# Kernel tuning notes

Hardware: AMD Instinct MI355X
Metric: run time of the kernel (lower is better)

The kernel has to match this reference:

```python
import jax, jax.numpy as jnp
import numpy as np

B, N, D, H, DK, DI = 64, 256, 1024, 8, 64, 2048
NEG = -1e9
SCALE = 1.0 / np.sqrt(DK).astype(np.float32)


def _ln(x, s, b, eps=1e-5):
    m = jnp.mean(x, axis=-1, keepdims=True)
    v = jnp.var(x, axis=-1, keepdims=True)
    return (x - m) * jax.lax.rsqrt(v + eps) * s + b


def _glat_basic(x, mask, npm, wq, wk, wv, wo, bo, ls1, lb1, w1, b1, w2, b2, ls2, lb2):
    # mask: [B,1,N,N] bool, True = blocked
    b, n, d = x.shape
    q = (x @ wq).reshape(b, n, H, DK).transpose(0, 2, 1, 3)  # [B,H,N,DK]
    k = (x @ wk).reshape(b, n, H, DK).transpose(0, 2, 1, 3)
    v = (x @ wv).reshape(b, n, H, DK).transpose(0, 2, 1, 3)
    scores = jnp.einsum('bhqd,bhkd->bhqk', q, k) * SCALE
    scores = jnp.where(mask, NEG, scores)
    attn = jax.nn.softmax(scores, axis=-1)
    out = jnp.einsum('bhqk,bhkd->bhqd', attn, v)
    out = out.transpose(0, 2, 1, 3).reshape(b, n, H * DK)
    out = out @ wo + bo
    out = _ln(out + x, ls1, lb1)           # attn residual + layernorm
    out = out * npm                         # non_pad_mask
    h = jax.nn.relu(out @ w1 + b1) @ w2 + b2
    out2 = _ln(h + out, ls2, lb2) * npm     # FFN residual + layernorm + mask
    return out2


def setup_inputs():
    key = jax.random.key(0)
    ks = jax.random.split(key, 40)
    p = lambda i, shape: jax.random.normal(ks[i], shape, jnp.float32) * 0.02
    inp = {
        'x': jax.random.normal(ks[0], (B, N, D), jnp.float32),
        'adj': jax.random.randint(ks[1], (B, N, N), 0, 2).astype(jnp.int32),
        'non_pad_mask': jnp.ones((B, N, 1), jnp.float32),
        'slf_attn_mask': jnp.zeros((B, N, N), jnp.int32),
    }
    i = 2
    for t in ('g', 'l'):
        inp[f'wq_{t}'] = p(i, (D, H * DK)); i += 1
        inp[f'wk_{t}'] = p(i, (D, H * DK)); i += 1
        inp[f'wv_{t}'] = p(i, (D, H * DK)); i += 1
        inp[f'wo_{t}'] = p(i, (H * DK, D)); i += 1
        inp[f'bo_{t}'] = jnp.zeros((D,), jnp.float32)
        inp[f'ln1s_{t}'] = jnp.ones((D,), jnp.float32)
        inp[f'ln1b_{t}'] = jnp.zeros((D,), jnp.float32)
        inp[f'w1_{t}'] = p(i, (D, DI)); i += 1
        inp[f'b1_{t}'] = jnp.zeros((DI,), jnp.float32)
        inp[f'w2_{t}'] = p(i, (DI, D)); i += 1
        inp[f'b2_{t}'] = jnp.zeros((D,), jnp.float32)
        inp[f'ln2s_{t}'] = jnp.ones((D,), jnp.float32)
        inp[f'ln2b_{t}'] = jnp.zeros((D,), jnp.float32)
    inp['fc_w'] = p(i, (2 * D, D)); i += 1
    inp['fc_b'] = jnp.zeros((D,), jnp.float32)
    return inp


def reference(x, adj, non_pad_mask, slf_attn_mask,
              wq_g, wk_g, wv_g, wo_g, bo_g, ln1s_g, ln1b_g, w1_g, b1_g, w2_g, b2_g, ln2s_g, ln2b_g,
              wq_l, wk_l, wv_l, wo_l, bo_l, ln1s_l, ln1b_l, w1_l, b1_l, w2_l, b2_l, ln2s_l, ln2b_l,
              fc_w, fc_b):
    pad_mask = (slf_attn_mask[:, None, :, :] != 0)            # [B,1,N,N]
    local_mask = pad_mask | (adj[:, None, :, :] == 0)         # local: only attend along edges
    x_g = _glat_basic(x, pad_mask, non_pad_mask,
                      wq_g, wk_g, wv_g, wo_g, bo_g, ln1s_g, ln1b_g,
                      w1_g, b1_g, w2_g, b2_g, ln2s_g, ln2b_g)
    x_l = _glat_basic(x, local_mask, non_pad_mask,
                      wq_l, wk_l, wv_l, wo_l, bo_l, ln1s_l, ln1b_l,
                      w1_l, b1_l, w2_l, b2_l, ln2s_l, ln2b_l)
    out = jnp.concatenate([x_g, x_l], axis=-1) @ fc_w + fc_b
    return out
```

## Files before the change

kernel.cpp:

```cpp
#include <hip/hip_runtime.h>


typedef unsigned short u16;
typedef unsigned long long u64;
typedef __bf16 bf16_t;
typedef bf16_t bf16x8 __attribute__((ext_vector_type(8)));
typedef float  f32x4  __attribute__((ext_vector_type(4)));
typedef u16    u16x8  __attribute__((ext_vector_type(8)));
typedef u16    u16x4  __attribute__((ext_vector_type(4)));

__device__ __forceinline__ float bf2f(u16 u){
  union { unsigned int i; float f; } c; c.i = ((unsigned int)u) << 16; return c.f;
}
__device__ __forceinline__ u16 f2bf(float f){
  union { float f; unsigned int u; } c; c.f = f;
  unsigned int u = c.u;
  unsigned int r = (u + 0x7fffu + ((u >> 16) & 1u)) >> 16;
  return (u16)r;
}

__device__ __forceinline__ void gl16(const u16* g, u16* l){
  __builtin_amdgcn_global_load_lds(
      (const __attribute__((address_space(1))) void*)g,
      (__attribute__((address_space(3))) void*)l, 16, 0, 0);
}

__global__ __launch_bounds__(256) void zero_out(float* out, int n){
  for (int i = blockIdx.x * 256 + threadIdx.x; i < n; i += 256 * 4096) out[i] = 0.f;
}

__global__ __launch_bounds__(256) void cvt_bf16(
    const float* __restrict__ in, u16* __restrict__ out)
{
  const size_t i = ((size_t)blockIdx.x * 256 + threadIdx.x) * 8;
  f32x4 a = *(const f32x4*)&in[i];
  f32x4 b = *(const f32x4*)&in[i + 4];
  u16x8 o;
  #pragma unroll
  for (int j = 0; j < 4; ++j){ o[j] = f2bf(a[j]); o[4+j] = f2bf(b[j]); }
  *(u16x8*)&out[i] = o;
}

__global__ __launch_bounds__(256) void transpose_w(
    const float* __restrict__ src, u16* __restrict__ dst, int K, int N, int dstOff)
{
  __shared__ u16 tile[32][33];
  const int bk = blockIdx.x * 32, bn = blockIdx.y * 32;
  const int t = threadIdx.x;
  const int r = t >> 5, c = t & 31;
  #pragma unroll
  for (int p = 0; p < 4; ++p)
    tile[r + p*8][c] = f2bf(src[(size_t)(bk + r + p*8) * N + bn + c]);
  __syncthreads();
  #pragma unroll
  for (int p = 0; p < 4; ++p)
    dst[(size_t)(dstOff + bn + r + p*8) * K + bk + c] = tile[c][r + p*8];
}

__global__ __launch_bounds__(256) void transpose_w3(
    const float* __restrict__ sA, const float* __restrict__ sB,
    const float* __restrict__ sC, u16* __restrict__ dst, int K, int N)
{
  __shared__ u16 tile[32][33];
  const float* src = blockIdx.z == 0 ? sA : (blockIdx.z == 1 ? sB : sC);
  const int dstOff = blockIdx.z * N;
  const int bk = blockIdx.x * 32, bn = blockIdx.y * 32;
  const int t = threadIdx.x;
  const int r = t >> 5, c = t & 31;
  #pragma unroll
  for (int p = 0; p < 4; ++p)
    tile[r + p*8][c] = f2bf(src[(size_t)(bk + r + p*8) * N + bn + c]);
  __syncthreads();
  #pragma unroll
  for (int p = 0; p < 4; ++p)
    dst[(size_t)(dstOff + bn + r + p*8) * K + bk + c] = tile[c][r + p*8];
}

template<int RELU, int OF32, int ACC>
__global__ __launch_bounds__(512, 2) void gemm256(
    const u16* __restrict__ A0, const u16* __restrict__ A1,
    int Astride, int ksplit,
    const u16* __restrict__ BT, int Bld, int M, int N, int K,
    const float* __restrict__ bias, void* __restrict__ outv, int out_ld)
{
  __shared__ u16 lds[2*32768];
  const int tid  = threadIdx.x;
  const int lane = tid & 63;
  const int wid  = tid >> 6;
  const int wm = wid >> 2, wn = wid & 3;
  const int l15 = lane & 15, l4 = lane >> 4;
  const int m0 = blockIdx.x * 256, n0 = blockIdx.y * 256;

  f32x4 acc[8][4];
  #pragma unroll
  for (int i = 0; i < 8; ++i)
    #pragma unroll
    for (int j = 0; j < 4; ++j)
      acc[i][j] = (f32x4){0.f, 0.f, 0.f, 0.f};

  const int s0 = tid, s1 = tid + 512;
  const int r0 = s0 >> 3, g0 = (s0 & 7) ^ (r0 & 7);
  const int r1 = s1 >> 3, g1 = (s1 & 7) ^ (r1 & 7);

  const int nt = K >> 6;

  auto stageA = [&](int kt, int h, int buf){
    const int kb = kt * 64;
    const u16* Ab = A0; int kl = kb;
    if (kb >= ksplit){ Ab = A1; kl = kb - ksplit; }
    u16* dst = &lds[buf*32768 + h*8192];
    gl16(&Ab[(size_t)(m0 + h*128 + r0) * Astride + kl + g0*8], &dst[s0*8]);
    gl16(&Ab[(size_t)(m0 + h*128 + r1) * Astride + kl + g1*8], &dst[s1*8]);
  };
  auto stageB = [&](int kt, int h, int buf){
    const int kb = kt * 64;
    u16* dst = &lds[buf*32768 + 16384 + h*8192];
    gl16(&BT[(size_t)(n0 + h*128 + r0) * Bld + kb + g0*8], &dst[s0*8]);
    gl16(&BT[(size_t)(n0 + h*128 + r1) * Bld + kb + g1*8], &dst[s1*8]);
  };
  auto lda = [&](int i, int kc, int buf) -> bf16x8 {
    const int r = wm*128 + i*16 + l15;
    const int c = (kc*4 + l4) ^ (r & 7);
    return *(const bf16x8*)&lds[buf*32768 + r*64 + c*8];
  };
  auto ldb = [&](int j, int kc, int buf) -> bf16x8 {
    const int r = wn*64 + j*16 + l15;
    const int c = (kc*4 + l4) ^ (r & 7);
    return *(const bf16x8*)&lds[buf*32768 + 16384 + r*64 + c*8];
  };

  stageA(0, 0, 0); stageA(0, 1, 0); stageB(0, 0, 0); stageB(0, 1, 0);

  for (int t = 0; t < nt; ++t){
    const int buf = t & 1, nbuf = buf ^ 1;
    const bool pf = (t + 1 < nt);
    if (pf){
      stageA(t+1, 0, nbuf);
      asm volatile("s_waitcnt vmcnt(2)" ::: "memory");
    } else {
      asm volatile("s_waitcnt vmcnt(0)" ::: "memory");
    }
    __builtin_amdgcn_sched_barrier(0);
    __builtin_amdgcn_s_barrier();
    __builtin_amdgcn_sched_barrier(0);

    bf16x8 a_[4][2], b_[2][2];
    #pragma unroll
    for (int i = 0; i < 4; ++i){ a_[i][0] = lda(i, 0, buf); a_[i][1] = lda(i, 1, buf); }
    #pragma unroll
    for (int j = 0; j < 2; ++j){ b_[j][0] = ldb(j, 0, buf); b_[j][1] = ldb(j, 1, buf); }
    if (pf) stageA(t+1, 1, nbuf);
    __builtin_amdgcn_s_setprio(1);
    #pragma unroll
    for (int i = 0; i < 4; ++i)
      #pragma unroll
      for (int j = 0; j < 2; ++j){
        acc[i][j] = __builtin_amdgcn_mfma_f32_16x16x32_bf16(a_[i][0], b_[j][0], acc[i][j], 0,0,0);
        acc[i][j] = __builtin_amdgcn_mfma_f32_16x16x32_bf16(a_[i][1], b_[j][1], acc[i][j], 0,0,0);
      }
    __builtin_amdgcn_s_setprio(0);
    #pragma unroll
    for (int j = 0; j < 2; ++j){ b_[j][0] = ldb(2+j, 0, buf); b_[j][1] = ldb(2+j, 1, buf); }
    if (pf) stageB(t+1, 0, nbuf);
    __builtin_amdgcn_s_setprio(1);
    #pragma unroll
    for (int i = 0; i < 4; ++i)
      #pragma unroll
      for (int j = 0; j < 2; ++j){
        acc[i][2+j] = __builtin_amdgcn_mfma_f32_16x16x32_bf16(a_[i][0], b_[j][0], acc[i][2+j], 0,0,0);
        acc[i][2+j] = __builtin_amdgcn_mfma_f32_16x16x32_bf16(a_[i][1], b_[j][1], acc[i][2+j], 0,0,0);
      }
    __builtin_amdgcn_s_setprio(0);
    #pragma unroll
    for (int i = 0; i < 4; ++i){ a_[i][0] = lda(4+i, 0, buf); a_[i][1] = lda(4+i, 1, buf); }
    if (pf) stageB(t+1, 1, nbuf);
    __builtin_amdgcn_s_setprio(1);
    #pragma unroll
    for (int i = 0; i < 4; ++i)
      #pragma unroll
      for (int j = 0; j < 2; ++j){
        acc[4+i][2+j] = __builtin_amdgcn_mfma_f32_16x16x32_bf16(a_[i][0], b_[j][0], acc[4+i][2+j], 0,0,0);
        acc[4+i][2+j] = __builtin_amdgcn_mfma_f32_16x16x32_bf16(a_[i][1], b_[j][1], acc[4+i][2+j], 0,0,0);
      }
    __builtin_amdgcn_s_setprio(0);
    #pragma unroll
    for (int j = 0; j < 2; ++j){ b_[j][0] = ldb(j, 0, buf); b_[j][1] = ldb(j, 1, buf); }
    __builtin_amdgcn_s_setprio(1);
    #pragma unroll
    for (int i = 0; i < 4; ++i)
      #pragma unroll
      for (int j = 0; j < 2; ++j){
        acc[4+i][j] = __builtin_amdgcn_mfma_f32_16x16x32_bf16(a_[i][0], b_[j][0], acc[4+i][j], 0,0,0);
        acc[4+i][j] = __builtin_amdgcn_mfma_f32_16x16x32_bf16(a_[i][1], b_[j][1], acc[4+i][j], 0,0,0);
      }
    __builtin_amdgcn_s_setprio(0);

    __builtin_amdgcn_sched_barrier(0);
    __builtin_amdgcn_s_barrier();
    __builtin_amdgcn_sched_barrier(0);
  }

  const int rb = m0 + wm*128 + l4*4;
  const int cb = n0 + wn*64 + l15;
  #pragma unroll
  for (int i = 0; i < 8; ++i){
    #pragma unroll
    for (int j = 0; j < 4; ++j){
      const int col = cb + j*16;
      const float badd = bias ? bias[col] : 0.f;
      #pragma unroll
      for (int r = 0; r < 4; ++r){
        const int row = rb + i*16 + r;
        float y = acc[i][j][r] + badd;
        if (RELU) y = y > 0.f ? y : 0.f;
        if (OF32){
          float* po = &((float*)outv)[(size_t)row * out_ld + col];
          if (ACC) y += *po;
          *po = y;
        } else {
          u16* po = &((u16*)outv)[(size_t)row * out_ld + col];
          if (ACC) y += bf2f(*po);
          *po = f2bf(y);
        }
      }
    }
  }
}

__global__ __launch_bounds__(256) void mask_pack(
    const int* __restrict__ slf, const int* __restrict__ adj,
    u64* __restrict__ mb_g, u64* __restrict__ mb_l)
{
  const int idx  = blockIdx.x * 4 + (threadIdx.x >> 6);
  const int lane = threadIdx.x & 63;
  const size_t mi = (size_t)(idx >> 2) * 256 + (size_t)(idx & 3) * 64 + lane;
  const bool g = slf[mi] != 0;
  const bool l = g || (adj[mi] == 0);
  const u64 bg = __ballot(g);
  const u64 bl = __ballot(l);
  if (lane == 0){ mb_g[idx] = bg; mb_l[idx] = bl; }
}

__global__ __launch_bounds__(256) void attn_mfma(
    const u16* __restrict__ qkv, const u64* __restrict__ mb,
    int boff, u16* __restrict__ out)
{
  __shared__ u16 kbuf[64*64];
  __shared__ u16 vtbuf[64*64];
  __shared__ u16 pbuf[4][32*64];

  const int b_loc = blockIdx.x >> 4;
  const int h     = (blockIdx.x >> 1) & 7;
  const int qt    = blockIdx.x & 1;
  const int b     = boff + b_loc;
  const int t     = threadIdx.x;
  const int w     = t >> 6, lane = t & 63;
  const int l15   = lane & 15, l4 = lane >> 4;

  bf16x8 qf[2][2];
  {
    const int rbase = b_loc*256 + qt*128 + w*32;
    #pragma unroll
    for (int i = 0; i < 2; ++i)
      #pragma unroll
      for (int kc = 0; kc < 2; ++kc)
        qf[i][kc] = *(const bf16x8*)&qkv[(size_t)(rbase + i*16 + l15)*1536 + h*64 + kc*32 + l4*8];
  }

  f32x4 acc_o[2][4];
  float m_[2][4], l_[2][4];
  #pragma unroll
  for (int i = 0; i < 2; ++i){
    #pragma unroll
    for (int j = 0; j < 4; ++j) acc_o[i][j] = (f32x4){0.f,0.f,0.f,0.f};
    #pragma unroll
    for (int r = 0; r < 4; ++r){ m_[i][r] = -1e30f; l_[i][r] = 0.f; }
  }

  for (int c = 0; c < 4; ++c){
    __syncthreads();
    {
      const int kr = t >> 2, dg = (t & 3) * 16;
      const size_t rbase = (size_t)(b_loc*256 + c*64 + kr)*1536 + h*64 + dg;
      u16x8 k0 = *(const u16x8*)&qkv[rbase + 512];
      u16x8 k1 = *(const u16x8*)&qkv[rbase + 512 + 8];
      u16x8 v0 = *(const u16x8*)&qkv[rbase + 1024];
      u16x8 v1 = *(const u16x8*)&qkv[rbase + 1024 + 8];
      const int sw = (kr & 7) << 3;
      *(u16x8*)&kbuf[kr*64 + (dg ^ sw)]       = k0;
      *(u16x8*)&kbuf[kr*64 + ((dg + 8) ^ sw)] = k1;
      #pragma unroll
      for (int e = 0; e < 8; ++e){
        const int d0 = dg + e, d1 = dg + 8 + e;
        vtbuf[d0*64 + (kr ^ ((d0 & 7) << 3))] = v0[e];
        vtbuf[d1*64 + (kr ^ ((d1 & 7) << 3))] = v1[e];
      }
    }
    __syncthreads();

    bf16x8 kfr[4][2];
    #pragma unroll
    for (int jb = 0; jb < 4; ++jb){
      const int key = jb*16 + l15;
      const int sw = (key & 7) << 3;
      #pragma unroll
      for (int kc = 0; kc < 2; ++kc)
        kfr[jb][kc] = *(const bf16x8*)&kbuf[key*64 + ((kc*32 + l4*8) ^ sw)];
    }
    f32x4 s_[2][4];
    #pragma unroll
    for (int i = 0; i < 2; ++i)
      #pragma unroll
      for (int jb = 0; jb < 4; ++jb){
        f32x4 a = (f32x4){0.f,0.f,0.f,0.f};
        a = __builtin_amdgcn_mfma_f32_16x16x32_bf16(qf[i][0], kfr[jb][0], a, 0,0,0);
        a = __builtin_amdgcn_mfma_f32_16x16x32_bf16(qf[i][1], kfr[jb][1], a, 0,0,0);
        s_[i][jb] = a;
      }

    #pragma unroll
    for (int i = 0; i < 2; ++i){
      #pragma unroll
      for (int r = 0; r < 4; ++r){
        const int prow = i*16 + l4*4 + r;
        const int qrow = qt*128 + w*32 + prow;
        const u64 bits = mb[((size_t)b*256 + qrow)*4 + c];
        float sv[4];
        #pragma unroll
        for (int jb = 0; jb < 4; ++jb){
          float xv = s_[i][jb][r] * 0.125f;
          if ((bits >> (jb*16 + l15)) & 1ull) xv = -1e9f;
          sv[jb] = xv;
        }
        float mx = fmaxf(fmaxf(sv[0], sv[1]), fmaxf(sv[2], sv[3]));
        #pragma unroll
        for (int d = 1; d < 16; d <<= 1)
          mx = fmaxf(mx, __shfl_xor(mx, d, 64));
        const float mnew = fmaxf(m_[i][r], mx);
        const float corr = __expf(m_[i][r] - mnew);
        m_[i][r] = mnew;
        float ps = 0.f;
        const int swp = (prow & 7) << 3;
        #pragma unroll
        for (int jb = 0; jb < 4; ++jb){
          const float p = __expf(sv[jb] - mnew);
          ps += p;
          pbuf[w][prow*64 + ((jb*16 + l15) ^ swp)] = f2bf(p);
        }
        #pragma unroll
        for (int d = 1; d < 16; d <<= 1)
          ps += __shfl_xor(ps, d, 64);
        l_[i][r] = l_[i][r] * corr + ps;
        #pragma unroll
        for (int j2 = 0; j2 < 4; ++j2) acc_o[i][j2][r] *= corr;
      }
    }

    bf16x8 vfr[4][2];
    #pragma unroll
    for (int j2 = 0; j2 < 4; ++j2){
      const int dim = j2*16 + l15;
      const int sw = (dim & 7) << 3;
      #pragma unroll
      for (int kc = 0; kc < 2; ++kc)
        vfr[j2][kc] = *(const bf16x8*)&vtbuf[dim*64 + ((kc*32 + l4*8) ^ sw)];
    }
    #pragma unroll
    for (int i = 0; i < 2; ++i){
      const int prow = i*16 + l15;
      const int swp = (prow & 7) << 3;
      bf16x8 pa0 = *(const bf16x8*)&pbuf[w][prow*64 + ((l4*8) ^ swp)];
      bf16x8 pa1 = *(const bf16x8*)&pbuf[w][prow*64 + ((32 + l4*8) ^ swp)];
      #pragma unroll
      for (int j2 = 0; j2 < 4; ++j2){
        acc_o[i][j2] = __builtin_amdgcn_mfma_f32_16x16x32_bf16(pa0, vfr[j2][0], acc_o[i][j2], 0,0,0);
        acc_o[i][j2] = __builtin_amdgcn_mfma_f32_16x16x32_bf16(pa1, vfr[j2][1], acc_o[i][j2], 0,0,0);
      }
    }
  }

  #pragma unroll
  for (int i = 0; i < 2; ++i){
    #pragma unroll
    for (int r = 0; r < 4; ++r){
      const int qrow = qt*128 + w*32 + i*16 + l4*4 + r;
      const float inv = 1.f / l_[i][r];
      const size_t ob = ((size_t)b*256 + qrow)*512 + h*64;
      #pragma unroll
      for (int j2 = 0; j2 < 4; ++j2)
        out[ob + j2*16 + l15] = f2bf(acc_o[i][j2][r] * inv);
    }
  }
}

template<int RF32>
__global__ __launch_bounds__(256) void ln_fused(
    const u16* a, const void* __restrict__ res,
    const float* __restrict__ sc, const float* __restrict__ bs,
    const float* __restrict__ npm, u16* out)
{
  const int w = threadIdx.x >> 6, lane = threadIdx.x & 63;
  const int row = blockIdx.x * 4 + w;
  const size_t bse = (size_t)row * 1024 + lane * 16;

  u16x8 av0 = *(const u16x8*)&a[bse];
  u16x8 av1 = *(const u16x8*)&a[bse + 8];
  float rv[16];
  if (RF32){
    const float* rp = (const float*)res + bse;
    #pragma unroll
    for (int j = 0; j < 16; j += 4){
      f32x4 q = *(const f32x4*)&rp[j];
      rv[j] = q[0]; rv[j+1] = q[1]; rv[j+2] = q[2]; rv[j+3] = q[3];
    }
  } else {
    const u16* rp = (const u16*)res + bse;
    u16x8 q0 = *(const u16x8*)rp;
    u16x8 q1 = *(const u16x8*)(rp + 8);
    #pragma unroll
    for (int j = 0; j < 8; ++j){ rv[j] = bf2f(q0[j]); rv[8+j] = bf2f(q1[j]); }
  }

  float vv[16]; float s = 0.f, sq = 0.f;
  #pragma unroll
  for (int j = 0; j < 8; ++j){
    vv[j]   = bf2f(av0[j]) + rv[j];
    vv[8+j] = bf2f(av1[j]) + rv[8+j];
  }
  #pragma unroll
  for (int j = 0; j < 16; ++j){ s += vv[j]; sq += vv[j]*vv[j]; }
  #pragma unroll
  for (int i = 1; i < 64; i <<= 1){
    s  += __shfl_xor(s,  i, 64);
    sq += __shfl_xor(sq, i, 64);
  }
  const float mean = s * (1.f/1024.f);
  const float var  = sq * (1.f/1024.f) - mean*mean;
  const float rstd = rsqrtf(var + 1e-5f);
  const float nm   = npm[row];

  u16x8 o0, o1;
  #pragma unroll
  for (int j = 0; j < 8; ++j){
    const int c0 = lane*16 + j, c1 = c0 + 8;
    o0[j] = f2bf(((vv[j]   - mean) * rstd * sc[c0] + bs[c0]) * nm);
    o1[j] = f2bf(((vv[8+j] - mean) * rstd * sc[c1] + bs[c1]) * nm);
  }
  *(u16x8*)&out[bse]     = o0;
  *(u16x8*)&out[bse + 8] = o1;
}

extern "C" void kernel_launch(void* const* d_in, const int* in_sizes, int n_in,
                              void* d_out, int out_size, void* d_ws, size_t ws_size,
                              hipStream_t stream)
{
  const size_t NEED = 58720256ull * 2ull;
  if (ws_size < NEED){
    zero_out<<<4096, 256, 0, stream>>>((float*)d_out, out_size);
    return;
  }

  const float* x   = (const float*)d_in[0];
  const int*   adj = (const int*)d_in[1];
  const float* npm = (const float*)d_in[2];
  const int*   slf = (const int*)d_in[3];
  const float* fcw = (const float*)d_in[30];
  const float* fcb = (const float*)d_in[31];

  u16* ws    = (u16*)d_ws;
  u16* wqkvT = ws;
  u16* woT   = ws + 1572864;
  u16* w1T   = ws + 2097152;
  u16* w2T   = ws + 4194304;
  u16* fcT   = ws + 6291456;
  u16* xbf   = ws + 8388608;
  u16* tmp   = ws + 8388608;
  u16* qkvh  = ws + 25165824;
  u16* ln1   = ws + 25165824;
  u16* xg    = ws + 41943040;

  u16* dout16 = (u16*)d_out;
  u16* attnb0 = dout16;
  u16* attnb1 = dout16 + 8388608;
  u16* hbufA  = dout16 + 16777216;
  u64* mb_g   = (u64*)(dout16 + 16777216);
  u64* mb_l   = mb_g + 65536;

  cvt_bf16<<<8192, 256, 0, stream>>>(x, xbf);
  mask_pack<<<16384, 256, 0, stream>>>(slf, adj, mb_g, mb_l);
  transpose_w<<<dim3(64, 32), 256, 0, stream>>>(fcw, fcT, 2048, 1024, 0);

  for (int L = 0; L < 2; ++L){
    const int bi = 4 + L*13;
    transpose_w3<<<dim3(32, 16, 3), 256, 0, stream>>>(
        (const float*)d_in[bi+0], (const float*)d_in[bi+1],
        (const float*)d_in[bi+2], wqkvT, 1024, 512);
    u16* attnb = L ? attnb1 : attnb0;
    for (int hf = 0; hf < 2; ++hf){
      const u16* xh = xbf + (size_t)hf*8192*1024;
      gemm256<0,0,0><<<dim3(32, 6), 512, 0, stream>>>(
          xh, xh, 1024, 1024, wqkvT, 1024, 8192, 1536, 1024, nullptr, qkvh, 1536);
      attn_mfma<<<512, 256, 0, stream>>>(qkvh, L ? mb_l : mb_g, hf*32, attnb);
    }
  }

  for (int L = 0; L < 2; ++L){
    const int bi = 4 + L*13;
    const float* bo  = (const float*)d_in[bi+4];
    const float* l1s = (const float*)d_in[bi+5];
    const float* l1b = (const float*)d_in[bi+6];
    const float* b1  = (const float*)d_in[bi+8];
    const float* b2  = (const float*)d_in[bi+10];
    const float* l2s = (const float*)d_in[bi+11];
    const float* l2b = (const float*)d_in[bi+12];

    transpose_w<<<dim3(16, 32), 256, 0, stream>>>((const float*)d_in[bi+3], woT, 512, 1024, 0);
    transpose_w<<<dim3(32, 64), 256, 0, stream>>>((const float*)d_in[bi+7], w1T, 1024, 2048, 0);
    transpose_w<<<dim3(64, 32), 256, 0, stream>>>((const float*)d_in[bi+9], w2T, 2048, 1024, 0);

    const u16* attnb = L ? attnb1 : attnb0;
    gemm256<0,0,0><<<dim3(64, 4), 512, 0, stream>>>(
        attnb, attnb, 512, 512, woT, 512, 16384, 1024, 512, bo, tmp, 1024);
    ln_fused<1><<<4096, 256, 0, stream>>>(tmp, x, l1s, l1b, npm, ln1);
    for (int hh = 0; hh < 2; ++hh){
      gemm256<1,0,0><<<dim3(64, 4), 512, 0, stream>>>(
          ln1, ln1, 1024, 1024, w1T + (size_t)hh*1024*1024, 1024,
          16384, 1024, 1024, b1 + hh*1024, hbufA, 1024);
      if (hh == 0)
        gemm256<0,0,0><<<dim3(64, 4), 512, 0, stream>>>(
            hbufA, hbufA, 1024, 1024, w2T, 2048, 16384, 1024, 1024, b2, tmp, 1024);
      else
        gemm256<0,0,1><<<dim3(64, 4), 512, 0, stream>>>(
            hbufA, hbufA, 1024, 1024, w2T + 1024, 2048, 16384, 1024, 1024,
            nullptr, tmp, 1024);
    }
    ln_fused<0><<<4096, 256, 0, stream>>>(tmp, ln1, l2s, l2b, npm, L ? tmp : xg);
  }

  gemm256<0,1,0><<<dim3(64, 4), 512, 0, stream>>>(
      xg, tmp, 1024, 1024, fcT, 2048, 16384, 1024, 2048, fcb, d_out, 1024);
}
```

Measured before the change: 796.2 us.

## Skip softmax rescale when max growth is small; merge FFN into full-width GEMMs

```diff
diff --git a/kernel.cpp b/kernel.cpp
--- a/kernel.cpp
+++ b/kernel.cpp
@@ -319,41 +319,75 @@
       }
 
     #pragma unroll
-    for (int i = 0; i < 2; ++i){
+    for (int i = 0; i < 2; ++i)
       #pragma unroll
       for (int r = 0; r < 4; ++r){
-        const int prow = i*16 + l4*4 + r;
-        const int qrow = qt*128 + w*32 + prow;
+        const int qrow = qt*128 + w*32 + i*16 + l4*4 + r;
         const u64 bits = mb[((size_t)b*256 + qrow)*4 + c];
-        float sv[4];
         #pragma unroll
         for (int jb = 0; jb < 4; ++jb){
           float xv = s_[i][jb][r] * 0.125f;
           if ((bits >> (jb*16 + l15)) & 1ull) xv = -1e9f;
-          sv[jb] = xv;
+          s_[i][jb][r] = xv;
         }
-        float mx = fmaxf(fmaxf(sv[0], sv[1]), fmaxf(sv[2], sv[3]));
+      }
+    float mxs[2][4];
+    bool okall = true;
+    #pragma unroll
+    for (int i = 0; i < 2; ++i)
+      #pragma unroll
+      for (int r = 0; r < 4; ++r){
+        float mx = fmaxf(fmaxf(s_[i][0][r], s_[i][1][r]),
+                         fmaxf(s_[i][2][r], s_[i][3][r]));
         #pragma unroll
         for (int d = 1; d < 16; d <<= 1)
           mx = fmaxf(mx, __shfl_xor(mx, d, 64));
-        const float mnew = fmaxf(m_[i][r], mx);
-        const float corr = __expf(m_[i][r] - mnew);
-        m_[i][r] = mnew;
-        float ps = 0.f;
-        const int swp = (prow & 7) << 3;
+        mxs[i][r] = mx;
+        okall = okall && (mx <= m_[i][r] + 8.f);
+      }
+    if (__all(okall)){
+      #pragma unroll
+      for (int i = 0; i < 2; ++i)
         #pragma unroll
-        for (int jb = 0; jb < 4; ++jb){
-          const float p = __expf(sv[jb] - mnew);
-          ps += p;
-          pbuf[w][prow*64 + ((jb*16 + l15) ^ swp)] = f2bf(p);
+        for (int r = 0; r < 4; ++r){
+          const int prow = i*16 + l4*4 + r;
+          const int swp = (prow & 7) << 3;
+          float ps = 0.f;
+          #pragma unroll
+          for (int jb = 0; jb < 4; ++jb){
+            const float p = __expf(s_[i][jb][r] - m_[i][r]);
+            ps += p;
+            pbuf[w][prow*64 + ((jb*16 + l15) ^ swp)] = f2bf(p);
+          }
+          #pragma unroll
+          for (int d = 1; d < 16; d <<= 1)
+            ps += __shfl_xor(ps, d, 64);
+          l_[i][r] += ps;
         }
+    } else {
+      #pragma unroll
+      for (int i = 0; i < 2; ++i)
         #pragma unroll
-        for (int d = 1; d < 16; d <<= 1)
-          ps += __shfl_xor(ps, d, 64);
-        l_[i][r] = l_[i][r] * corr + ps;
-        #pragma unroll
-        for (int j2 = 0; j2 < 4; ++j2) acc_o[i][j2][r] *= corr;
-      }
+        for (int r = 0; r < 4; ++r){
+          const int prow = i*16 + l4*4 + r;
+          const float mnew = fmaxf(m_[i][r], mxs[i][r]);
+          const float corr = __expf(m_[i][r] - mnew);
+          m_[i][r] = mnew;
+          float ps = 0.f;
+          const int swp = (prow & 7) << 3;
+          #pragma unroll
+          for (int jb = 0; jb < 4; ++jb){
+            const float p = __expf(s_[i][jb][r] - mnew);
+            ps += p;
+            pbuf[w][prow*64 + ((jb*16 + l15) ^ swp)] = f2bf(p);
+          }
+          #pragma unroll
+          for (int d = 1; d < 16; d <<= 1)
+            ps += __shfl_xor(ps, d, 64);
+          l_[i][r] = l_[i][r] * corr + ps;
+          #pragma unroll
+          for (int j2 = 0; j2 < 4; ++j2) acc_o[i][j2][r] *= corr;
+        }
     }
 
     bf16x8 vfr[4][2];
@@ -474,15 +508,15 @@
   u16* w2T   = ws + 4194304;
   u16* fcT   = ws + 6291456;
   u16* xbf   = ws + 8388608;
-  u16* tmp   = ws + 8388608;
+  u16* tmp0  = ws + 8388608;
   u16* qkvh  = ws + 25165824;
   u16* ln1   = ws + 25165824;
-  u16* xg    = ws + 41943040;
+  u16* tmp1  = ws + 41943040;
 
   u16* dout16 = (u16*)d_out;
   u16* attnb0 = dout16;
   u16* attnb1 = dout16 + 8388608;
-  u16* hbufA  = dout16 + 16777216;
+  u16* hbuf   = dout16;
   u64* mb_g   = (u64*)(dout16 + 16777216);
   u64* mb_l   = mb_g + 65536;
 
@@ -504,39 +538,36 @@
     }
   }
 
+  transpose_w<<<dim3(16, 32), 256, 0, stream>>>((const float*)d_in[4+3], woT, 512, 1024, 0);
+  gemm256<0,0,0><<<dim3(64, 4), 512, 0, stream>>>(
+      attnb0, attnb0, 512, 512, woT, 512, 16384, 1024, 512,
+      (const float*)d_in[4+4], tmp0, 1024);
+  transpose_w<<<dim3(16, 32), 256, 0, stream>>>((const float*)d_in[17+3], woT, 512, 1024, 0);
+  gemm256<0,0,0><<<dim3(64, 4), 512, 0, stream>>>(
+      attnb1, attnb1, 512, 512, woT, 512, 16384, 1024, 512,
+      (const float*)d_in[17+4], tmp1, 1024);
+
   for (int L = 0; L < 2; ++L){
     const int bi = 4 + L*13;
-    const float* bo  = (const float*)d_in[bi+4];
     const float* l1s = (const float*)d_in[bi+5];
     const float* l1b = (const float*)d_in[bi+6];
     const float* b1  = (const float*)d_in[bi+8];
     const float* b2  = (const float*)d_in[bi+10];
     const float* l2s = (const float*)d_in[bi+11];
     const float* l2b = (const float*)d_in[bi+12];
-
-    transpose_w<<<dim3(16, 32), 256, 0, stream>>>((const float*)d_in[bi+3], woT, 512, 1024, 0);
+    u16* tmpL = L ? tmp1 : tmp0;
+
     transpose_w<<<dim3(32, 64), 256, 0, stream>>>((const float*)d_in[bi+7], w1T, 1024, 2048, 0);
     transpose_w<<<dim3(64, 32), 256, 0, stream>>>((const float*)d_in[bi+9], w2T, 2048, 1024, 0);
 
-    const u16* attnb = L ? attnb1 : attnb0;
+    ln_fused<1><<<4096, 256, 0, stream>>>(tmpL, x, l1s, l1b, npm, ln1);
+    gemm256<1,0,0><<<dim3(64, 8), 512, 0, stream>>>(
+        ln1, ln1, 1024, 1024, w1T, 1024, 16384, 2048, 1024, b1, hbuf, 2048);
     gemm256<0,0,0><<<dim3(64, 4), 512, 0, stream>>>(
-        attnb, attnb, 512, 512, woT, 512, 16384, 1024, 512, bo, tmp, 1024);
-    ln_fused<1><<<4096, 256, 0, stream>>>(tmp, x, l1s, l1b, npm, ln1);
-    for (int hh = 0; hh < 2; ++hh){
-      gemm256<1,0,0><<<dim3(64, 4), 512, 0, stream>>>(
-          ln1, ln1, 1024, 1024, w1T + (size_t)hh*1024*1024, 1024,
-          16384, 1024, 1024, b1 + hh*1024, hbufA, 1024);
-      if (hh == 0)
-        gemm256<0,0,0><<<dim3(64, 4), 512, 0, stream>>>(
-            hbufA, hbufA, 1024, 1024, w2T, 2048, 16384, 1024, 1024, b2, tmp, 1024);
-      else
-        gemm256<0,0,1><<<dim3(64, 4), 512, 0, stream>>>(
-            hbufA, hbufA, 1024, 1024, w2T + 1024, 2048, 16384, 1024, 1024,
-            nullptr, tmp, 1024);
-    }
-    ln_fused<0><<<4096, 256, 0, stream>>>(tmp, ln1, l2s, l2b, npm, L ? tmp : xg);
+        hbuf, hbuf, 2048, 2048, w2T, 2048, 16384, 1024, 2048, b2, tmpL, 1024);
+    ln_fused<0><<<4096, 256, 0, stream>>>(tmpL, ln1, l2s, l2b, npm, tmpL);
   }
 
   gemm256<0,1,0><<<dim3(64, 4), 512, 0, stream>>>(
-      xg, tmp, 1024, 1024, fcT, 2048, 16384, 1024, 2048, fcb, d_out, 1024);
-}
+      tmp0, tmp1, 1024, 1024, fcT, 2048, 16384, 1024, 2048, fcb, d_out, 1024);
+}
```

Result: faster. 733.2 us (-7.9%).
